# Kernel optimization log

Measured on AMD Instinct MI355X. Metric: run time of the kernel, lower is better.

Reference implementation:

```python
import jax, jax.numpy as jnp
import numpy as np

N_NODES = 100000
N_EDGES = 1600000
IN_F = 128
HID = 16
NEG_SLOPE = 0.2


def setup_inputs() -> dict:
    key = jax.random.key(0)
    ks = jax.random.split(key, 12)
    x = jax.random.normal(ks[0], (N_NODES, IN_F), dtype=jnp.float32)
    edge_index = jax.random.randint(ks[1], (2, N_EDGES), 0, N_NODES, dtype=jnp.int32)
    s1 = 1.0 / np.sqrt(IN_F)
    s2 = 1.0 / np.sqrt(2 * HID)
    # layer 1: heads=2, out=16, concat -> 32
    W1 = jax.random.normal(ks[2], (IN_F, 2 * HID), dtype=jnp.float32) * s1
    a_src1 = jax.random.normal(ks[3], (2, HID), dtype=jnp.float32) * s2
    a_dst1 = jax.random.normal(ks[4], (2, HID), dtype=jnp.float32) * s2
    b1 = jnp.zeros((2 * HID,), dtype=jnp.float32)
    # layer 2: heads=1, out=1
    W2 = jax.random.normal(ks[5], (2 * HID, 1), dtype=jnp.float32) * s2
    a_src2 = jax.random.normal(ks[6], (1, 1), dtype=jnp.float32)
    a_dst2 = jax.random.normal(ks[7], (1, 1), dtype=jnp.float32)
    b2 = jnp.zeros((1,), dtype=jnp.float32)
    return {"x": x, "edge_index": edge_index, "W1": W1, "a_src1": a_src1,
            "a_dst1": a_dst1, "b1": b1, "W2": W2, "a_src2": a_src2,
            "a_dst2": a_dst2, "b2": b2}


def gat_conv(x, src, dst, W, a_src, a_dst, bias, heads, out_ch, concat):
    # PyG GATConv: linear proj, per-edge leaky-relu score, segment softmax over
    # incoming edges (dst), scatter-add aggregation. Self loops already in src/dst.
    n = x.shape[0]
    h = (x @ W).reshape(n, heads, out_ch)                      # [N,H,C]
    alpha_s = (h * a_src[None]).sum(-1)                        # [N,H]
    alpha_d = (h * a_dst[None]).sum(-1)                        # [N,H]
    e = jax.nn.leaky_relu(alpha_s[src] + alpha_d[dst], NEG_SLOPE)  # [E,H]
    m = jax.lax.stop_gradient(jax.ops.segment_max(e, dst, num_segments=n))
    ex = jnp.exp(e - m[dst])
    denom = jax.ops.segment_sum(ex, dst, num_segments=n)       # [N,H]
    alpha = ex / (denom[dst] + 1e-16)                          # [E,H]
    out = jax.ops.segment_sum(alpha[..., None] * h[src], dst, num_segments=n)  # [N,H,C]
    out = out.reshape(n, heads * out_ch) if concat else out.mean(axis=1)
    return out + bias


def reference(x, edge_index, W1, a_src1, a_dst1, b1, W2, a_src2, a_dst2, b2):
    n = x.shape[0]
    loop = jnp.arange(n, dtype=edge_index.dtype)
    src = jnp.concatenate([edge_index[0], loop])
    dst = jnp.concatenate([edge_index[1], loop])
    h = jax.nn.elu(gat_conv(x, src, dst, W1, a_src1, a_dst1, b1, 2, HID, True))
    out = gat_conv(h, src, dst, W2, a_src2, a_dst2, b2, 1, 1, False)
    return out
```

## Files before the change

### kernel.cpp

```cpp
#include <hip/hip_runtime.h>
#include <math.h>

#define IN_F 128
#define C1 32
#define NEG 0.2f
#define BSZ 256
#define CAP 4992
#define EPB 2048
#define TPW 2

typedef _Float16 h16;
typedef _Float16 h16x2 __attribute__((ext_vector_type(2)));
typedef _Float16 h16x4 __attribute__((ext_vector_type(4)));
typedef _Float16 h16x8 __attribute__((ext_vector_type(8)));
typedef float f32x4 __attribute__((ext_vector_type(4)));

__device__ __forceinline__ float leaky(float x) { return x >= 0.f ? x : NEG * x; }

__global__ __launch_bounds__(256)
void k_fat(const float* __restrict__ x, const float* __restrict__ W1,
           const float* __restrict__ a_s, const float* __restrict__ a_d,
           h16* __restrict__ h1h, float* __restrict__ as1,
           float* __restrict__ ad1, int N,
           const int* __restrict__ ei, int E, int ET, int nbk,
           int* __restrict__ bcnt, int* __restrict__ ebuf, int nproj) {
    __shared__ int smem[5120];
    int t = threadIdx.x;
    if ((int)blockIdx.x < nproj) {
        int wid = t >> 6, lane = t & 63;
        int q = lane >> 4, r = lane & 15;
        h16x8 Bf[2][4];
        #pragma unroll
        for (int ct = 0; ct < 2; ++ct)
            #pragma unroll
            for (int kc = 0; kc < 4; ++kc)
                #pragma unroll
                for (int j = 0; j < 8; ++j)
                    Bf[ct][kc][j] = (h16)W1[(kc * 32 + q * 8 + j) * C1 + ct * 16 + r];
        float a_s0 = a_s[r], a_s1v = a_s[16 + r];
        float a_d0 = a_d[r], a_d1v = a_d[16 + r];
        #pragma unroll
        for (int tt = 0; tt < TPW; ++tt) {
            int tile = (blockIdx.x * 4 + wid) * TPW + tt;
            int m0 = tile << 4;
            if (m0 >= N) break;
            int row = m0 + r; if (row >= N) row = N - 1;
            const float* xr = x + (size_t)row * IN_F + q * 8;
            f32x4 acc0 = {0.f, 0.f, 0.f, 0.f};
            f32x4 acc1 = {0.f, 0.f, 0.f, 0.f};
            #pragma unroll
            for (int kc = 0; kc < 4; ++kc) {
                float4 xa = *(const float4*)(xr + kc * 32);
                float4 xb = *(const float4*)(xr + kc * 32 + 4);
                h16x8 A;
                A[0] = (h16)xa.x; A[1] = (h16)xa.y; A[2] = (h16)xa.z; A[3] = (h16)xa.w;
                A[4] = (h16)xb.x; A[5] = (h16)xb.y; A[6] = (h16)xb.z; A[7] = (h16)xb.w;
                acc0 = __builtin_amdgcn_mfma_f32_16x16x32_f16(A, Bf[0][kc], acc0, 0, 0, 0);
                acc1 = __builtin_amdgcn_mfma_f32_16x16x32_f16(A, Bf[1][kc], acc1, 0, 0, 0);
            }
            #pragma unroll
            for (int reg = 0; reg < 4; ++reg) {
                int node = m0 + q * 4 + reg;
                bool vld = node < N;
                float h0 = acc0[reg], h1 = acc1[reg];
                if (vld) {
                    h1h[(size_t)node * C1 + r]      = (h16)h0;
                    h1h[(size_t)node * C1 + 16 + r] = (h16)h1;
                }
                float s0 = h0 * a_s0, s1 = h1 * a_s1v;
                float d0 = h0 * a_d0, d1 = h1 * a_d1v;
                s0 += __shfl_xor(s0, 1); s0 += __shfl_xor(s0, 2); s0 += __shfl_xor(s0, 4); s0 += __shfl_xor(s0, 8);
                s1 += __shfl_xor(s1, 1); s1 += __shfl_xor(s1, 2); s1 += __shfl_xor(s1, 4); s1 += __shfl_xor(s1, 8);
                d0 += __shfl_xor(d0, 1); d0 += __shfl_xor(d0, 2); d0 += __shfl_xor(d0, 4); d0 += __shfl_xor(d0, 8);
                d1 += __shfl_xor(d1, 1); d1 += __shfl_xor(d1, 2); d1 += __shfl_xor(d1, 4); d1 += __shfl_xor(d1, 8);
                if (vld && r == 0) {
                    *(float2*)&as1[node * 2] = make_float2(s0, s1);
                    *(float2*)&ad1[node * 2] = make_float2(d0, d1);
                }
            }
        }
    } else {
        int* hist = smem;
        int* lcur = hist + 512;
        int2* ecache = (int2*)(lcur + 512);
        int bid = blockIdx.x - nproj;
        hist[t] = 0; hist[t + 256] = 0;
        __syncthreads();
        int i0 = bid * EPB, i1 = min(ET, i0 + EPB);
        for (int i = i0 + t; i < i1; i += 256) {
            int s, d;
            if (i < E) { s = ei[i]; d = ei[E + i]; } else { s = d = i - E; }
            ecache[i - i0] = make_int2(s, d);
            atomicAdd(&hist[d >> 8], 1);
        }
        __syncthreads();
        for (int b = t; b < nbk; b += 256) {
            int h = hist[b];
            int base = h ? atomicAdd(&bcnt[b], h) : 0;
            lcur[b] = b * CAP + base;
        }
        __syncthreads();
        for (int i = i0 + t; i < i1; i += 256) {
            int2 e = ecache[i - i0];
            int bkt = e.y >> 8;
            int pos = atomicAdd(&lcur[bkt], 1);
            if (pos < (bkt + 1) * CAP)
                ebuf[pos] = (e.x << 8) | (e.y & 255);
        }
    }
}

__global__ __launch_bounds__(256)
void k_bcsr(const int* __restrict__ bcnt, const int* __restrict__ ebuf,
            int N, int nbk, int ET,
            const float* __restrict__ as1, const float* __restrict__ ad1,
            int* __restrict__ off, int2* __restrict__ csr2) {
    __shared__ int deg[256];
    __shared__ int cur[256];
    __shared__ float adl[512];
    __shared__ int red[4];
    int b = blockIdx.x, t = threadIdx.x;
    int part = 0;
    for (int k = t; k < b; k += 256) part += min(bcnt[k], CAP);
    part += __shfl_xor(part, 1);  part += __shfl_xor(part, 2);
    part += __shfl_xor(part, 4);  part += __shfl_xor(part, 8);
    part += __shfl_xor(part, 16); part += __shfl_xor(part, 32);
    if ((t & 63) == 0) red[t >> 6] = part;
    int cnt = min(bcnt[b], CAP);
    int ebase = b * CAP;
    int n0 = b * BSZ;
    deg[t] = 0;
    if (n0 + t < N) ((float2*)adl)[t] = ((const float2*)ad1)[n0 + t];
    __syncthreads();
    int fbase = red[0] + red[1] + red[2] + red[3];
    if (b == nbk - 1 && t == 0) off[N] = fbase + cnt;
    for (int i = t; i < cnt; i += 256)
        atomicAdd(&deg[ebuf[ebase + i] & 255], 1);
    __syncthreads();
    int v = deg[t];
    __syncthreads();
    for (int o = 1; o < 256; o <<= 1) {
        int xv = (t >= o) ? deg[t - o] : 0; __syncthreads();
        deg[t] += xv; __syncthreads();
    }
    int excl = deg[t] - v;
    if (n0 + t < N) off[n0 + t] = fbase + excl;
    cur[t] = fbase + excl;
    __syncthreads();
    for (int i = t; i < cnt; i += 256) {
        int e = ebuf[ebase + i];
        int dl = e & 255;
        int s = e >> 8;
        float2 asv = ((const float2*)as1)[s];
        float w0 = __expf(leaky(asv.x + adl[dl * 2 + 0]));
        float w1 = __expf(leaky(asv.y + adl[dl * 2 + 1]));
        h16x2 wp = { (h16)w0, (h16)w1 };
        int p = atomicAdd(&cur[dl], 1);
        int2 rec; rec.x = s; rec.y = *(int*)&wp;
        csr2[p] = rec;
    }
}

__global__ __launch_bounds__(256)
void k_l1agg(const int* __restrict__ off, const int2* __restrict__ csr2,
             const h16* __restrict__ h1h, const float* __restrict__ b1,
             const float* __restrict__ W2, float* __restrict__ p2, int N) {
    int t = threadIdx.x;
    int node = blockIdx.x * 32 + (t >> 3);
    if (node >= N) return;
    int l = t & 7;
    int c0 = l * 4;
    int head = l >> 2;
    float den = 0.f, a0 = 0.f, a1 = 0.f, a2 = 0.f, a3 = 0.f;
    int j0 = off[node], j1 = off[node + 1];
    for (int j = j0; j < j1; j += 4) {
        #pragma unroll
        for (int k = 0; k < 4; ++k) {
            int jj = j + k;
            bool valid = jj < j1;
            jj = valid ? jj : j0;
            int2 e = csr2[jj];
            int s = e.x;
            h16x2 wv = *(h16x2*)&e.y;
            float w = valid ? (float)(head ? wv.y : wv.x) : 0.f;
            h16x4 hv = *(const h16x4*)(h1h + ((size_t)s << 5) + c0);
            den += w;
            a0 = fmaf(w, (float)hv.x, a0);
            a1 = fmaf(w, (float)hv.y, a1);
            a2 = fmaf(w, (float)hv.z, a2);
            a3 = fmaf(w, (float)hv.w, a3);
        }
    }
    float inv = 1.f / (den + 1e-16f);
    float o, val = 0.f;
    o = a0 * inv + b1[c0 + 0]; o = o > 0.f ? o : expm1f(o); val = fmaf(o, W2[c0 + 0], val);
    o = a1 * inv + b1[c0 + 1]; o = o > 0.f ? o : expm1f(o); val = fmaf(o, W2[c0 + 1], val);
    o = a2 * inv + b1[c0 + 2]; o = o > 0.f ? o : expm1f(o); val = fmaf(o, W2[c0 + 2], val);
    o = a3 * inv + b1[c0 + 3]; o = o > 0.f ? o : expm1f(o); val = fmaf(o, W2[c0 + 3], val);
    val += __shfl_xor(val, 1); val += __shfl_xor(val, 2); val += __shfl_xor(val, 4);
    if (l == 0) p2[node] = val;
}

__global__ void k_l2(const int* __restrict__ off, const int2* __restrict__ csr2,
                     const float* __restrict__ p2, const float* __restrict__ as2,
                     const float* __restrict__ ad2, const float* __restrict__ b2,
                     float* __restrict__ out, int N) {
    int i = blockIdx.x * blockDim.x + threadIdx.x;
    if (i >= N) return;
    float A = as2[0];
    float Bc = ad2[0] * p2[i];
    float den = 0.f, num = 0.f;
    int j0 = off[i], j1 = off[i + 1];
    for (int j = j0; j < j1; j += 4) {
        #pragma unroll
        for (int k = 0; k < 4; ++k) {
            int jj = j + k;
            bool valid = jj < j1;
            int s = csr2[valid ? jj : j0].x;
            float ps = p2[s];
            float w = valid ? __expf(leaky(fmaf(ps, A, Bc))) : 0.f;
            den += w;
            num = fmaf(w, ps, num);
        }
    }
    out[i] = num / (den + 1e-16f) + b2[0];
}

extern "C" void kernel_launch(void* const* d_in, const int* in_sizes, int n_in,
                              void* d_out, int out_size, void* d_ws, size_t ws_size,
                              hipStream_t stream) {
    const float* x    = (const float*)d_in[0];
    const int*   ei   = (const int*)d_in[1];
    const float* W1   = (const float*)d_in[2];
    const float* a_s1 = (const float*)d_in[3];
    const float* a_d1 = (const float*)d_in[4];
    const float* b1   = (const float*)d_in[5];
    const float* W2   = (const float*)d_in[6];
    const float* a_s2 = (const float*)d_in[7];
    const float* a_d2 = (const float*)d_in[8];
    const float* b2   = (const float*)d_in[9];
    float* out = (float*)d_out;

    const int N  = in_sizes[0] / IN_F;
    const int E  = in_sizes[1] / 2;
    const int ET = E + N;
    const int nbk = (N + BSZ - 1) / BSZ;

    float* w   = (float*)d_ws;
    float* as1 = w; w += (size_t)2 * N;
    float* ad1 = w; w += (size_t)2 * N;
    float* p2  = w; w += (size_t)N;
    h16* h1h   = (h16*)w;
    w += (size_t)16 * N;
    int* iw     = (int*)w;
    int* bcnt   = iw; iw += 512;
    int* off    = iw; iw += (N + 1);
    iw += (iw - (int*)d_ws) & 1;
    int2* csr2  = (int2*)iw; iw += (size_t)2 * ET;
    int* ebuf   = iw; iw += (size_t)nbk * CAP;

    const int B = 256;
    const int ntile = (N + 15) / 16;
    const int nproj = (ntile + 4 * TPW - 1) / (4 * TPW);
    const int nblkA = (ET + EPB - 1) / EPB;

    hipMemsetAsync(bcnt, 0, 512 * sizeof(int), stream);
    k_fat  <<<nproj + nblkA, B, 0, stream>>>(x, W1, a_s1, a_d1, h1h, as1, ad1, N,
                                             ei, E, ET, nbk, bcnt, ebuf, nproj);
    k_bcsr <<<nbk, B, 0, stream>>>(bcnt, ebuf, N, nbk, ET, as1, ad1, off, csr2);
    k_l1agg<<<(N + 31) / 32, B, 0, stream>>>(off, csr2, h1h, b1, W2, p2, N);
    k_l2   <<<(N + B - 1) / B, B, 0, stream>>>(off, csr2, p2, a_s2, a_d2, b2, out, N);
}
```

Baseline: 199.9 us.

## Fuse CSR build with layer-1 aggregation using shared-memory edge list

Merges the bucketed CSR construction and layer-1 aggregation into one 512-thread kernel per 256-node bucket. Edge records (source plus fp16 weights) are kept in a roughly 40KB shared-memory list instead of a global int2 CSR, and only source indices go out to a compact int CSR for layer 2. This cuts a kernel launch and the global write and re-read of the weighted CSR. In exchange, shared-memory use per block is large, which limits occupancy, and only 512 threads per bucket run the gather-heavy aggregation. off[N] is now set to ET, which differs from the old value if buckets overflow CAP.

Result: faster. 182.7 us (-8.6%).

```diff
diff --git a/kernel.cpp b/kernel.cpp
--- a/kernel.cpp
+++ b/kernel.cpp
@@ -110,98 +110,106 @@
     }
 }
 
-__global__ __launch_bounds__(256)
-void k_bcsr(const int* __restrict__ bcnt, const int* __restrict__ ebuf,
+__global__ __launch_bounds__(512)
+void k_bagg(const int* __restrict__ bcnt, const int* __restrict__ ebuf,
             int N, int nbk, int ET,
             const float* __restrict__ as1, const float* __restrict__ ad1,
-            int* __restrict__ off, int2* __restrict__ csr2) {
-    __shared__ int deg[256];
-    __shared__ int cur[256];
+            const float* __restrict__ b1, const float* __restrict__ W2,
+            const h16* __restrict__ h1h, int* __restrict__ off,
+            int* __restrict__ csr1, float* __restrict__ p2) {
+    __shared__ int2 elist[CAP];
+    __shared__ int deg[256], sst[256], cur[256];
     __shared__ float adl[512];
-    __shared__ int red[4];
+    __shared__ int red[8];
     int b = blockIdx.x, t = threadIdx.x;
+    int cnt = min(bcnt[b], CAP);
+    int ebase = b * CAP;
+    int n0 = b * BSZ;
     int part = 0;
-    for (int k = t; k < b; k += 256) part += min(bcnt[k], CAP);
+    for (int k = t; k < b; k += 512) part += min(bcnt[k], CAP);
     part += __shfl_xor(part, 1);  part += __shfl_xor(part, 2);
     part += __shfl_xor(part, 4);  part += __shfl_xor(part, 8);
     part += __shfl_xor(part, 16); part += __shfl_xor(part, 32);
     if ((t & 63) == 0) red[t >> 6] = part;
-    int cnt = min(bcnt[b], CAP);
-    int ebase = b * CAP;
-    int n0 = b * BSZ;
-    deg[t] = 0;
-    if (n0 + t < N) ((float2*)adl)[t] = ((const float2*)ad1)[n0 + t];
-    __syncthreads();
-    int fbase = red[0] + red[1] + red[2] + red[3];
-    if (b == nbk - 1 && t == 0) off[N] = fbase + cnt;
-    for (int i = t; i < cnt; i += 256)
+    if (t < 256) {
+        deg[t] = 0;
+        int n = n0 + t;
+        float2 v = (n < N) ? ((const float2*)ad1)[n] : make_float2(0.f, 0.f);
+        adl[t * 2] = v.x; adl[t * 2 + 1] = v.y;
+    }
+    __syncthreads();
+    int fbase = red[0] + red[1] + red[2] + red[3] + red[4] + red[5] + red[6] + red[7];
+    if (b == nbk - 1 && t == 0) off[N] = ET;
+    for (int i = t; i < cnt; i += 512)
         atomicAdd(&deg[ebuf[ebase + i] & 255], 1);
     __syncthreads();
-    int v = deg[t];
+    int v = (t < 256) ? deg[t] : 0;
     __syncthreads();
     for (int o = 1; o < 256; o <<= 1) {
-        int xv = (t >= o) ? deg[t - o] : 0; __syncthreads();
-        deg[t] += xv; __syncthreads();
-    }
-    int excl = deg[t] - v;
-    if (n0 + t < N) off[n0 + t] = fbase + excl;
-    cur[t] = fbase + excl;
-    __syncthreads();
-    for (int i = t; i < cnt; i += 256) {
+        int xv = (t >= o && t < 256) ? deg[t - o] : 0;
+        __syncthreads();
+        if (t < 256) deg[t] += xv;
+        __syncthreads();
+    }
+    if (t < 256) {
+        int excl = deg[t] - v;
+        sst[t] = excl; cur[t] = excl;
+        if (n0 + t < N) off[n0 + t] = fbase + excl;
+    }
+    __syncthreads();
+    for (int i = t; i < cnt; i += 512) {
         int e = ebuf[ebase + i];
-        int dl = e & 255;
-        int s = e >> 8;
+        int dl = e & 255, s = e >> 8;
         float2 asv = ((const float2*)as1)[s];
         float w0 = __expf(leaky(asv.x + adl[dl * 2 + 0]));
         float w1 = __expf(leaky(asv.y + adl[dl * 2 + 1]));
         h16x2 wp = { (h16)w0, (h16)w1 };
         int p = atomicAdd(&cur[dl], 1);
         int2 rec; rec.x = s; rec.y = *(int*)&wp;
-        csr2[p] = rec;
-    }
-}
-
-__global__ __launch_bounds__(256)
-void k_l1agg(const int* __restrict__ off, const int2* __restrict__ csr2,
-             const h16* __restrict__ h1h, const float* __restrict__ b1,
-             const float* __restrict__ W2, float* __restrict__ p2, int N) {
-    int t = threadIdx.x;
-    int node = blockIdx.x * 32 + (t >> 3);
-    if (node >= N) return;
-    int l = t & 7;
-    int c0 = l * 4;
-    int head = l >> 2;
-    float den = 0.f, a0 = 0.f, a1 = 0.f, a2 = 0.f, a3 = 0.f;
-    int j0 = off[node], j1 = off[node + 1];
-    for (int j = j0; j < j1; j += 4) {
-        #pragma unroll
-        for (int k = 0; k < 4; ++k) {
-            int jj = j + k;
-            bool valid = jj < j1;
-            jj = valid ? jj : j0;
-            int2 e = csr2[jj];
-            int s = e.x;
-            h16x2 wv = *(h16x2*)&e.y;
-            float w = valid ? (float)(head ? wv.y : wv.x) : 0.f;
-            h16x4 hv = *(const h16x4*)(h1h + ((size_t)s << 5) + c0);
-            den += w;
-            a0 = fmaf(w, (float)hv.x, a0);
-            a1 = fmaf(w, (float)hv.y, a1);
-            a2 = fmaf(w, (float)hv.z, a2);
-            a3 = fmaf(w, (float)hv.w, a3);
-        }
-    }
-    float inv = 1.f / (den + 1e-16f);
-    float o, val = 0.f;
-    o = a0 * inv + b1[c0 + 0]; o = o > 0.f ? o : expm1f(o); val = fmaf(o, W2[c0 + 0], val);
-    o = a1 * inv + b1[c0 + 1]; o = o > 0.f ? o : expm1f(o); val = fmaf(o, W2[c0 + 1], val);
-    o = a2 * inv + b1[c0 + 2]; o = o > 0.f ? o : expm1f(o); val = fmaf(o, W2[c0 + 2], val);
-    o = a3 * inv + b1[c0 + 3]; o = o > 0.f ? o : expm1f(o); val = fmaf(o, W2[c0 + 3], val);
-    val += __shfl_xor(val, 1); val += __shfl_xor(val, 2); val += __shfl_xor(val, 4);
-    if (l == 0) p2[node] = val;
-}
-
-__global__ void k_l2(const int* __restrict__ off, const int2* __restrict__ csr2,
+        elist[p] = rec;
+        csr1[fbase + p] = s;
+    }
+    __syncthreads();
+    int l = t & 7, slot = t >> 3, c0 = l * 4, head = l >> 2;
+    float b1l[4] = { b1[c0], b1[c0 + 1], b1[c0 + 2], b1[c0 + 3] };
+    float w2l[4] = { W2[c0], W2[c0 + 1], W2[c0 + 2], W2[c0 + 3] };
+    #pragma unroll
+    for (int pass = 0; pass < 4; ++pass) {
+        int dl = pass * 64 + slot;
+        int node = n0 + dl;
+        if (node >= N) break;
+        int j0 = sst[dl], j1 = deg[dl];
+        float den = 0.f, a0 = 0.f, a1 = 0.f, a2 = 0.f, a3 = 0.f;
+        for (int j = j0; j < j1; j += 4) {
+            #pragma unroll
+            for (int k = 0; k < 4; ++k) {
+                int jj = j + k;
+                bool valid = jj < j1;
+                jj = valid ? jj : j0;
+                int2 e = elist[jj];
+                int s = e.x;
+                h16x2 wv = *(h16x2*)&e.y;
+                float w = valid ? (float)(head ? wv.y : wv.x) : 0.f;
+                h16x4 hv = *(const h16x4*)(h1h + ((size_t)s << 5) + c0);
+                den += w;
+                a0 = fmaf(w, (float)hv.x, a0);
+                a1 = fmaf(w, (float)hv.y, a1);
+                a2 = fmaf(w, (float)hv.z, a2);
+                a3 = fmaf(w, (float)hv.w, a3);
+            }
+        }
+        float inv = 1.f / (den + 1e-16f);
+        float o, val = 0.f;
+        o = a0 * inv + b1l[0]; o = o > 0.f ? o : expm1f(o); val = fmaf(o, w2l[0], val);
+        o = a1 * inv + b1l[1]; o = o > 0.f ? o : expm1f(o); val = fmaf(o, w2l[1], val);
+        o = a2 * inv + b1l[2]; o = o > 0.f ? o : expm1f(o); val = fmaf(o, w2l[2], val);
+        o = a3 * inv + b1l[3]; o = o > 0.f ? o : expm1f(o); val = fmaf(o, w2l[3], val);
+        val += __shfl_xor(val, 1); val += __shfl_xor(val, 2); val += __shfl_xor(val, 4);
+        if (l == 0) p2[node] = val;
+    }
+}
+
+__global__ void k_l2(const int* __restrict__ off, const int* __restrict__ csr1,
                      const float* __restrict__ p2, const float* __restrict__ as2,
                      const float* __restrict__ ad2, const float* __restrict__ b2,
                      float* __restrict__ out, int N) {
@@ -216,7 +224,7 @@
         for (int k = 0; k < 4; ++k) {
             int jj = j + k;
             bool valid = jj < j1;
-            int s = csr2[valid ? jj : j0].x;
+            int s = csr1[valid ? jj : j0];
             float ps = p2[s];
             float w = valid ? __expf(leaky(fmaf(ps, A, Bc))) : 0.f;
             den += w;
@@ -255,8 +263,7 @@
     int* iw     = (int*)w;
     int* bcnt   = iw; iw += 512;
     int* off    = iw; iw += (N + 1);
-    iw += (iw - (int*)d_ws) & 1;
-    int2* csr2  = (int2*)iw; iw += (size_t)2 * ET;
+    int* csr1   = iw; iw += ET;
     int* ebuf   = iw; iw += (size_t)nbk * CAP;
 
     const int B = 256;
@@ -265,9 +272,9 @@
     const int nblkA = (ET + EPB - 1) / EPB;
 
     hipMemsetAsync(bcnt, 0, 512 * sizeof(int), stream);
-    k_fat  <<<nproj + nblkA, B, 0, stream>>>(x, W1, a_s1, a_d1, h1h, as1, ad1, N,
-                                             ei, E, ET, nbk, bcnt, ebuf, nproj);
-    k_bcsr <<<nbk, B, 0, stream>>>(bcnt, ebuf, N, nbk, ET, as1, ad1, off, csr2);
-    k_l1agg<<<(N + 31) / 32, B, 0, stream>>>(off, csr2, h1h, b1, W2, p2, N);
-    k_l2   <<<(N + B - 1) / B, B, 0, stream>>>(off, csr2, p2, a_s2, a_d2, b2, out, N);
-}
+    k_fat <<<nproj + nblkA, B, 0, stream>>>(x, W1, a_s1, a_d1, h1h, as1, ad1, N,
+                                            ei, E, ET, nbk, bcnt, ebuf, nproj);
+    k_bagg<<<nbk, 512, 0, stream>>>(bcnt, ebuf, N, nbk, ET, as1, ad1, b1, W2,
+                                    h1h, off, csr1, p2);
+    k_l2  <<<(N + B - 1) / B, B, 0, stream>>>(off, csr1, p2, a_s2, a_d2, b2, out, N);
+}
```
